# Performance work log

Measured on AMD Instinct MI355X. Metric: run time of the kernel, lower is better.

Reference implementation:

```python
import jax, jax.numpy as jnp
import numpy as np

B, S, IN, H, OUT, L = 64, 512, 512, 1024, 512, 2


def setup_inputs() -> dict:
    key = jax.random.key(0)
    ks = jax.random.split(key, 12)
    s_in = 1.0 / np.sqrt(IN)
    s_h = 1.0 / np.sqrt(H)
    inp = {
        "x": jax.random.normal(ks[0], (B, S, IN), dtype=jnp.float32),
        "h0": jnp.zeros((B, L, H), dtype=jnp.float32),
        # layer 0: gates stacked [z; r; g] along first axis
        "Wx0": jax.random.uniform(ks[1], (3 * H, IN), minval=-s_in, maxval=s_in),
        "Wh0": jax.random.uniform(ks[2], (3 * H, H), minval=-s_h, maxval=s_h),
        "bh0": jax.random.uniform(ks[3], (3 * H,), minval=-s_h, maxval=s_h),
        # layer 1 (input dim is H)
        "Wx1": jax.random.uniform(ks[4], (3 * H, H), minval=-s_h, maxval=s_h),
        "Wh1": jax.random.uniform(ks[5], (3 * H, H), minval=-s_h, maxval=s_h),
        "bh1": jax.random.uniform(ks[6], (3 * H,), minval=-s_h, maxval=s_h),
        # output projection fc_hy
        "Why": jax.random.uniform(ks[7], (OUT, H), minval=-s_h, maxval=s_h),
        "by": jax.random.uniform(ks[8], (OUT,), minval=-s_h, maxval=s_h),
    }
    return inp


def _gru_layer(x, h_init, Wx, Wh, bh):
    """x: [B,S,D], h_init: [B,H]. Returns (ys [B,S,H], h_final [B,H])."""
    # Batch the input-side projections for all timesteps at once.
    xp = jnp.einsum("bsd,gd->bsg", x, Wx)  # [B,S,3H]
    xz, xr, xg = jnp.split(xp, 3, axis=-1)
    Whz, Whr, Whg = jnp.split(Wh, 3, axis=0)
    bhz, bhr, bhg = jnp.split(bh, 3, axis=0)

    def step(h, xs):
        xz_t, xr_t, xg_t = xs  # each [B,H]
        z = jax.nn.sigmoid(xz_t + h @ Whz.T + bhz)
        r = jax.nn.sigmoid(xr_t + h @ Whr.T + bhr)
        g = jnp.tanh(xg_t + (r * h) @ Whg.T + bhg)
        h_new = z * h + (1.0 - z) * g
        return h_new, h_new

    # time-major scan
    xs = (xz.transpose(1, 0, 2), xr.transpose(1, 0, 2), xg.transpose(1, 0, 2))
    h_final, ys = jax.lax.scan(step, h_init, xs)
    return ys.transpose(1, 0, 2), h_final  # [B,S,H], [B,H]


def reference(x, h0, Wx0, Wh0, bh0, Wx1, Wh1, bh1, Why, by):
    # dropout rate is 0 -> dropout is identity
    y0, hf0 = _gru_layer(x, h0[:, 0, :], Wx0, Wh0, bh0)
    y1, hf1 = _gru_layer(y0, h0[:, 1, :], Wx1, Wh1, bh1)
    layer_output = jnp.einsum("bsh,oh->bso", y1, Why) + by  # [B,S,OUT]
    hidden_state = jnp.stack([hf0, hf1], axis=1)  # [B,L,H]
    return layer_output, jax.lax.stop_gradient(hidden_state)
```

## Files before the change

kernel.cpp:

```cpp
#include <hip/hip_runtime.h>
#include <hip/hip_bf16.h>

#define B_   64
#define S_   512
#define IN_  512
#define H_   1024
#define OUT_ 512
#define H3_  3072
#define TC_  32
#define TCL2 5
#define NCHUNK (S_ / TC_)
#define MC_  (B_ * TC_)
#define NROW (B_ * S_)

#define NBLK 512
#define NTHR 128
#define EXN  32768
#define FPAD 16
#define STAGE_OFF 0
#define HOWN_OFF  32768
#define ZOWN_OFF  33920
#define SMEM_BYTES 35072

typedef float f32x4 __attribute__((ext_vector_type(4)));
typedef short bf16x8 __attribute__((ext_vector_type(8)));
typedef unsigned int u32;
typedef u32 u32x4 __attribute__((ext_vector_type(4)));

struct ChainArgs {
  const float* xp;
  const __hip_bfloat16* Wh;
  float* hf;
  u32* hbuf;
  u32* rhbuf;
  u32* fA;
  u32* fB;
  __hip_bfloat16* y;
  u32 baseA, baseB;
  int t0;
  int layer;
  int active;
  int stagger;
};

__device__ __forceinline__ u32 f2bf_bits(float v) {
  union { __hip_bfloat16 b; unsigned short s; } cv;
  cv.b = __float2bfloat16(v);
  return (u32)cv.s;
}

__device__ __forceinline__ void coh_st(u32* p, u32 v) {
  __hip_atomic_store(p, v, __ATOMIC_RELAXED, __HIP_MEMORY_SCOPE_AGENT);
}
__device__ __forceinline__ u32 coh_ld(const u32* p) {
  return __hip_atomic_load(p, __ATOMIC_RELAXED, __HIP_MEMORY_SCOPE_AGENT);
}

__device__ __forceinline__ void waitflags(const u32* f, int rgbase, u32 target) {
  const u32* my = f + (size_t)(rgbase + (threadIdx.x & 63)) * FPAD;
  int it = 0;
  while (true) {
    u32 v = coh_ld(my);
    if (__all((int)(v >= target))) break;
    if (it < 2) {
      __builtin_amdgcn_s_sleep(2);
    } else {
      __builtin_amdgcn_s_sleep(8);
    }
    ++it;
  }
  __builtin_amdgcn_sched_barrier(0);
}

__device__ __forceinline__ void stage_ex(const u32* __restrict__ src, char* stage, int tid,
                                         int rg) {
  u32x4 v[16];
#pragma unroll
  for (int i = 0; i < 16; ++i) {
    int c4 = tid + i * NTHR;
    int cgp = c4 >> 5;
    int s = c4 & 31;
    const u32* p = src + (((size_t)(cgp * 4 + rg) * 16 + (s >> 1)) * 8 + (s & 1) * 4);
    asm volatile("global_load_dwordx4 %0, %1, off sc0 sc1" : "=v"(v[i]) : "v"(p));
  }
  asm volatile("s_waitcnt vmcnt(0)" ::: "memory");
#pragma unroll
  for (int i = 0; i < 16; ++i) {
    int c4 = tid + i * NTHR;
    int cgp = c4 >> 5;
    int s = c4 & 31;
    int r = s >> 1;
    *(u32x4*)(stage + r * 2048 + (((cgp * 32 + (s & 1) * 16)) ^ ((r & 7) << 4))) = v[i];
  }
}

__global__ __launch_bounds__(256) void cast_f32_to_bf16(const float* __restrict__ in,
                                                        __hip_bfloat16* __restrict__ out,
                                                        int n4) {
  int i = blockIdx.x * 256 + threadIdx.x;
  if (i >= n4) return;
  float4 v = ((const float4*)in)[i];
  out[4 * i + 0] = __float2bfloat16(v.x);
  out[4 * i + 1] = __float2bfloat16(v.y);
  out[4 * i + 2] = __float2bfloat16(v.z);
  out[4 * i + 3] = __float2bfloat16(v.w);
}

__global__ __launch_bounds__(256) void gather_cast_x(const float* __restrict__ x,
                                                     __hip_bfloat16* __restrict__ out, int t0) {
  int i = blockIdx.x * 256 + threadIdx.x;
  int e = i * 4;
  int b = e >> 14;
  int rem = e & 16383;
  float4 v = *(const float4*)(x + (size_t)b * (S_ * IN_) + (size_t)t0 * IN_ + rem);
  out[e + 0] = __float2bfloat16(v.x);
  out[e + 1] = __float2bfloat16(v.y);
  out[e + 2] = __float2bfloat16(v.z);
  out[e + 3] = __float2bfloat16(v.w);
}

template <bool REMAP>
__global__ __launch_bounds__(256) void gemm_nt_bias(const __hip_bfloat16* __restrict__ A,
                                                    const __hip_bfloat16* __restrict__ Bm,
                                                    const float* __restrict__ bias,
                                                    float* __restrict__ C, int M, int N, int K,
                                                    int t0) {
  const int lane = threadIdx.x & 63;
  const int w = threadIdx.x >> 6;
  const int wr = w >> 1, wc = w & 1;
  const int row0 = blockIdx.y * 128 + wr * 64;
  const int col0 = blockIdx.x * 128 + wc * 64;
  const int kl = (lane >> 4) * 8;
  const int m16 = lane & 15;
  f32x4 acc[4][4] = {};
  for (int k0 = 0; k0 < K; k0 += 32) {
    bf16x8 a[4], b[4];
#pragma unroll
    for (int i = 0; i < 4; ++i)
      a[i] = *(const bf16x8*)(A + (size_t)(row0 + i * 16 + m16) * K + k0 + kl);
#pragma unroll
    for (int j = 0; j < 4; ++j)
      b[j] = *(const bf16x8*)(Bm + (size_t)(col0 + j * 16 + m16) * K + k0 + kl);
#pragma unroll
    for (int i = 0; i < 4; ++i)
#pragma unroll
      for (int j = 0; j < 4; ++j)
        acc[i][j] = __builtin_amdgcn_mfma_f32_16x16x32_bf16(a[i], b[j], acc[i][j], 0, 0, 0);
  }
  const int rsub = (lane >> 4) * 4;
#pragma unroll
  for (int i = 0; i < 4; ++i) {
    int row = row0 + i * 16 + rsub;
#pragma unroll
    for (int j = 0; j < 4; ++j) {
      int col = col0 + j * 16 + m16;
      float bv = bias[col];
#pragma unroll
      for (int r = 0; r < 4; ++r) {
        int rr = row + r;
        int crow = REMAP ? ((rr >> TCL2) * S_ + t0 + (rr & (TC_ - 1))) : rr;
        C[(size_t)crow * N + col] = acc[i][j][r] + bv;
      }
    }
  }
}

__device__ __forceinline__ void chain_scan(const ChainArgs& ca, const float* __restrict__ h0,
                                           float* __restrict__ hid_out, char* smem, int bx) {
  char* stage = smem + STAGE_OFF;
  float* h_own = (float*)(smem + HOWN_OFF);
  float* z_own = (float*)(smem + ZOWN_OFF);

  const int tid = threadIdx.x;
  const int lane = tid & 63;
  const int w = tid >> 6;
  const int rg = bx >> 6;
  const int cg = bx & 63;
  const int fid = bx;
  const int rgbase = rg * 64;
  const int m16 = lane & 15;
  const int kl = (lane >> 4) * 8;
  const int rsub = (lane >> 4) * 4;
  const int swzA = (m16 & 7) << 4;

  const float* xp = ca.xp;
  const __hip_bfloat16* Wh = ca.Wh;
  u32* hbuf = ca.hbuf;
  u32* rhbuf = ca.rhbuf;
  u32* flagA = ca.fA;
  u32* flagB = ca.fB;
  const u32 baseA = ca.baseA, baseB = ca.baseB;
  const int t0 = ca.t0, layer = ca.layer;

  for (int i = 0; i < ca.stagger; ++i) __builtin_amdgcn_s_sleep(16);

  {
    int row = tid >> 3, pp = tid & 7;
    int col = cg * 16 + pp * 2;
    int grow = rg * 16 + row;
    float v0, v1;
    if (t0 == 0) {
      v0 = h0[((size_t)grow * 2 + layer) * H_ + col];
      v1 = h0[((size_t)grow * 2 + layer) * H_ + col + 1];
      coh_st(hbuf + EXN + (((size_t)(cg * 4 + rg) * 16 + row) * 8 + pp),
             f2bf_bits(v0) | (f2bf_bits(v1) << 16));
    } else {
      v0 = ca.hf[grow * H_ + col];
      v1 = ca.hf[grow * H_ + col + 1];
    }
    h_own[row * 17 + pp * 2] = v0;
    h_own[row * 17 + pp * 2 + 1] = v1;
  }
  asm volatile("s_waitcnt vmcnt(0)" ::: "memory");
  __syncthreads();
  if (tid == 0) coh_st(flagB + (size_t)fid * FPAD, baseB + 1);

  for (int t = 0; t < TC_; ++t) {
    const int par = t & 1;
    const int colA = cg * 16 + m16 + ((w == 1) ? H_ : 0);
    float xpv[4], xpg[4];
#pragma unroll
    for (int j = 0; j < 4; ++j) {
      int grow = rg * 16 + rsub + j;
      xpv[j] = xp[((size_t)(grow * TC_ + t)) * H3_ + colA];
    }
    if (w == 0) {
#pragma unroll
      for (int j = 0; j < 4; ++j) {
        int grow = rg * 16 + rsub + j;
        xpg[j] = xp[((size_t)(grow * TC_ + t)) * H3_ + 2 * H_ + cg * 16 + m16];
      }
    }

    waitflags(flagB, rgbase, baseB + 1 + t);
    stage_ex(hbuf + (par ^ 1) * EXN, stage, tid, rg);
    __syncthreads();
    {
      f32x4 acc0 = {}, acc1 = {};
      const char* abase = stage + m16 * 2048;
      const __hip_bfloat16* Bb = Wh + (size_t)colA * H_;
#pragma unroll
      for (int k0 = 0; k0 < H_; k0 += 64) {
        bf16x8 a0 = *(const bf16x8*)(abase + (((k0 + kl) * 2) ^ swzA));
        bf16x8 a1 = *(const bf16x8*)(abase + (((k0 + 32 + kl) * 2) ^ swzA));
        bf16x8 b0 = *(const bf16x8*)(Bb + k0 + kl);
        bf16x8 b1 = *(const bf16x8*)(Bb + k0 + 32 + kl);
        acc0 = __builtin_amdgcn_mfma_f32_16x16x32_bf16(a0, b0, acc0, 0, 0, 0);
        acc1 = __builtin_amdgcn_mfma_f32_16x16x32_bf16(a1, b1, acc1, 0, 0, 0);
      }
      if (w == 0) {
#pragma unroll
        for (int j = 0; j < 4; ++j) {
          float pre = acc0[j] + acc1[j] + xpv[j];
          z_own[(rsub + j) * 17 + m16] = 1.f / (1.f + expf(-pre));
        }
      } else {
#pragma unroll
        for (int j = 0; j < 4; ++j) {
          int lr = rsub + j;
          float pre = acc0[j] + acc1[j] + xpv[j];
          float s = 1.f / (1.f + expf(-pre));
          float rh = s * h_own[lr * 17 + m16];
          u32 bits = f2bf_bits(rh);
          u32 pair = bits | (((u32)__shfl_down((int)bits, 1)) << 16);
          if ((m16 & 1) == 0)
            coh_st(rhbuf + par * EXN + (((size_t)(cg * 4 + rg) * 16 + lr) * 8 + (m16 >> 1)),
                   pair);
        }
        asm volatile("s_waitcnt vmcnt(0)" ::: "memory");
      }
    }
    __syncthreads();
    if (tid == 0) coh_st(flagA + (size_t)fid * FPAD, baseA + t + 1);

    waitflags(flagA, rgbase, baseA + t + 1);
    stage_ex(rhbuf + par * EXN, stage, tid, rg);
    __syncthreads();
    if (w == 0) {
      f32x4 acc0 = {}, acc1 = {};
      const char* abase = stage + m16 * 2048;
      const __hip_bfloat16* Bb = Wh + (size_t)(2 * H_ + cg * 16 + m16) * H_;
#pragma unroll
      for (int k0 = 0; k0 < H_; k0 += 64) {
        bf16x8 a0 = *(const bf16x8*)(abase + (((k0 + kl) * 2) ^ swzA));
        bf16x8 a1 = *(const bf16x8*)(abase + (((k0 + 32 + kl) * 2) ^ swzA));
        bf16x8 b0 = *(const bf16x8*)(Bb + k0 + kl);
        bf16x8 b1 = *(const bf16x8*)(Bb + k0 + 32 + kl);
        acc0 = __builtin_amdgcn_mfma_f32_16x16x32_bf16(a0, b0, acc0, 0, 0, 0);
        acc1 = __builtin_amdgcn_mfma_f32_16x16x32_bf16(a1, b1, acc1, 0, 0, 0);
      }
#pragma unroll
      for (int j = 0; j < 4; ++j) {
        int lr = rsub + j;
        float pre = acc0[j] + acc1[j] + xpg[j];
        float gg = tanhf(pre);
        float zz = z_own[lr * 17 + m16];
        float hv = h_own[lr * 17 + m16];
        float hn = zz * hv + (1.f - zz) * gg;
        h_own[lr * 17 + m16] = hn;
        u32 bits = f2bf_bits(hn);
        u32 pair = bits | (((u32)__shfl_down((int)bits, 1)) << 16);
        if ((m16 & 1) == 0)
          coh_st(hbuf + par * EXN + (((size_t)(cg * 4 + rg) * 16 + lr) * 8 + (m16 >> 1)), pair);
        ca.y[((size_t)((rg * 16 + lr) * TC_ + t)) * H_ + cg * 16 + m16] = __float2bfloat16(hn);
      }
      asm volatile("s_waitcnt vmcnt(0)" ::: "memory");
    }
    __syncthreads();
    if (tid == 0) coh_st(flagB + (size_t)fid * FPAD, baseB + t + 2);
  }

  {
    int row = tid >> 3, pp = tid & 7;
    int col = cg * 16 + pp * 2;
    int grow = rg * 16 + row;
    float v0 = h_own[row * 17 + pp * 2];
    float v1 = h_own[row * 17 + pp * 2 + 1];
    ca.hf[grow * H_ + col] = v0;
    ca.hf[grow * H_ + col + 1] = v1;
    if (t0 + TC_ == S_) {
      hid_out[((size_t)grow * 2 + layer) * H_ + col] = v0;
      hid_out[((size_t)grow * 2 + layer) * H_ + col + 1] = v1;
    }
  }
}

__global__ __launch_bounds__(NTHR) void gru_scan_fused(ChainArgs a0, ChainArgs a1,
                                                       const float* __restrict__ h0,
                                                       float* __restrict__ hid_out) {
  extern __shared__ char smem[];
  if (blockIdx.x < 256) {
    if (!a0.active) return;
    chain_scan(a0, h0, hid_out, smem, blockIdx.x);
  } else {
    if (!a1.active) return;
    chain_scan(a1, h0, hid_out, smem, blockIdx.x - 256);
  }
}

extern "C" void kernel_launch(void* const* d_in, const int* in_sizes, int n_in,
                              void* d_out, int out_size, void* d_ws, size_t ws_size,
                              hipStream_t stream) {
  const float* x   = (const float*)d_in[0];
  const float* h0  = (const float*)d_in[1];
  const float* Wx0 = (const float*)d_in[2];
  const float* Wh0 = (const float*)d_in[3];
  const float* bh0 = (const float*)d_in[4];
  const float* Wx1 = (const float*)d_in[5];
  const float* Wh1 = (const float*)d_in[6];
  const float* bh1 = (const float*)d_in[7];
  const float* Why = (const float*)d_in[8];
  const float* by  = (const float*)d_in[9];
  float* out = (float*)d_out;
  float* hid_out = out + (size_t)NROW * OUT_;

  (void)hipFuncSetAttribute((const void*)gru_scan_fused,
                            hipFuncAttributeMaxDynamicSharedMemorySize, SMEM_BYTES);

  char* ws = (char*)d_ws;
  size_t off = 0;
  auto alloc = [&](size_t bytes) {
    char* p = ws + off;
    off += (bytes + 255) & ~(size_t)255;
    return p;
  };
  __hip_bfloat16* wx0b = (__hip_bfloat16*)alloc((size_t)H3_ * IN_ * 2);
  __hip_bfloat16* wh0b = (__hip_bfloat16*)alloc((size_t)H3_ * H_ * 2);
  __hip_bfloat16* wx1b = (__hip_bfloat16*)alloc((size_t)H3_ * H_ * 2);
  __hip_bfloat16* wh1b = (__hip_bfloat16*)alloc((size_t)H3_ * H_ * 2);
  __hip_bfloat16* whyb = (__hip_bfloat16*)alloc((size_t)OUT_ * H_ * 2);
  float* h_f32_0 = (float*)alloc((size_t)B_ * H_ * 4);
  float* h_f32_1 = (float*)alloc((size_t)B_ * H_ * 4);
  u32* hbuf_0  = (u32*)alloc((size_t)2 * EXN * 4);
  u32* hbuf_1  = (u32*)alloc((size_t)2 * EXN * 4);
  u32* rhbuf_0 = (u32*)alloc((size_t)2 * EXN * 4);
  u32* rhbuf_1 = (u32*)alloc((size_t)2 * EXN * 4);
  __hip_bfloat16* x_bfc = (__hip_bfloat16*)alloc((size_t)MC_ * IN_ * 2);
  __hip_bfloat16* y0buf = (__hip_bfloat16*)alloc((size_t)MC_ * H_ * 2);
  __hip_bfloat16* y1buf = (__hip_bfloat16*)alloc((size_t)MC_ * H_ * 2);
  float* xp0buf = (float*)alloc((size_t)MC_ * H3_ * 4);
  float* xp1buf = (float*)alloc((size_t)MC_ * H3_ * 4);
  u32* flags    = (u32*)alloc(4 * 256 * FPAD * 4);
  (void)ws_size;

  (void)hipMemsetAsync(flags, 0, 4 * 256 * FPAD * 4, stream);

  auto cast = [&](const float* in, __hip_bfloat16* o, size_t n) {
    cast_f32_to_bf16<<<dim3((unsigned)((n / 4 + 255) / 256)), dim3(256), 0, stream>>>(in, o,
                                                                                     (int)(n / 4));
  };
  cast(Wx0, wx0b, (size_t)H3_ * IN_);
  cast(Wh0, wh0b, (size_t)H3_ * H_);
  cast(Wx1, wx1b, (size_t)H3_ * H_);
  cast(Wh1, wh1b, (size_t)H3_ * H_);
  cast(Why, whyb, (size_t)OUT_ * H_);

  u32* fA0 = flags;
  u32* fB0 = flags + 256 * FPAD;
  u32* fA1 = flags + 512 * FPAD;
  u32* fB1 = flags + 768 * FPAD;

  auto mkchain = [&](int layer, int chunk, int active) {
    ChainArgs ca;
    int cc = chunk < 0 ? 0 : chunk;
    ca.xp = layer == 0 ? xp0buf : xp1buf;
    ca.Wh = layer == 0 ? wh0b : wh1b;
    ca.hf = layer == 0 ? h_f32_0 : h_f32_1;
    ca.hbuf = layer == 0 ? hbuf_0 : hbuf_1;
    ca.rhbuf = layer == 0 ? rhbuf_0 : rhbuf_1;
    ca.fA = layer == 0 ? fA0 : fA1;
    ca.fB = layer == 0 ? fB0 : fB1;
    ca.y = layer == 0 ? y0buf : y1buf;
    ca.baseA = (u32)cc * TC_;
    ca.baseB = (u32)cc * (TC_ + 1);
    ca.t0 = cc * TC_;
    ca.layer = layer;
    ca.active = active;
    ca.stagger = (layer == 1) ? 14 : 0;
    return ca;
  };

  gather_cast_x<<<dim3(MC_ * IN_ / 4 / 256), dim3(256), 0, stream>>>(x, x_bfc, 0);
  gemm_nt_bias<false><<<dim3(H3_ / 128, MC_ / 128), dim3(256), 0, stream>>>(
      x_bfc, wx0b, bh0, xp0buf, MC_, H3_, IN_, 0);

  for (int c = 0; c <= NCHUNK; ++c) {
    ChainArgs a0 = mkchain(0, c, c < NCHUNK ? 1 : 0);
    ChainArgs a1 = mkchain(1, c - 1, c > 0 ? 1 : 0);
    {
      void* args[] = {(void*)&a0, (void*)&a1, (void*)&h0, (void*)&hid_out};
      hipError_t e = hipLaunchCooperativeKernel((void*)gru_scan_fused, dim3(NBLK), dim3(NTHR),
                                                args, SMEM_BYTES, stream);
      if (e != hipSuccess) {
        (void)hipGetLastError();
        gru_scan_fused<<<dim3(NBLK), dim3(NTHR), SMEM_BYTES, stream>>>(a0, a1, h0, hid_out);
      }
    }
    if (c < NCHUNK) {
      gemm_nt_bias<false><<<dim3(H3_ / 128, MC_ / 128), dim3(256), 0, stream>>>(
          y0buf, wx1b, bh1, xp1buf, MC_, H3_, H_, 0);
    }
    if (c + 1 < NCHUNK) {
      gather_cast_x<<<dim3(MC_ * IN_ / 4 / 256), dim3(256), 0, stream>>>(x, x_bfc, (c + 1) * TC_);
      gemm_nt_bias<false><<<dim3(H3_ / 128, MC_ / 128), dim3(256), 0, stream>>>(
          x_bfc, wx0b, bh0, xp0buf, MC_, H3_, IN_, 0);
    }
    if (c > 0) {
      gemm_nt_bias<true><<<dim3(OUT_ / 128, MC_ / 128), dim3(256), 0, stream>>>(
          y1buf, whyb, by, out, MC_, OUT_, H_, (c - 1) * TC_);
    }
  }
}
```

Before: 10.59 ms.

## Consolidate GRU scan into fewer, wider blocks with 64 columns each

Each scan block now owns 64 hidden columns with 8 waves (4 z-gate, 4 r-gate) instead of 16 columns with 2 waves, so 128 blocks replace 512. This cuts the number of cross-block flags each step must poll from 64 to 16 per row group, and amortises staging of the shared hidden state across more columns per block. The exchange buffer layout, staging loop and flag indexing are rewritten to match. In exchange, only 128 CUs are used per step and each block carries more MFMA work serially.

```diff
diff --git a/kernel.cpp b/kernel.cpp
--- a/kernel.cpp
+++ b/kernel.cpp
@@ -13,14 +13,14 @@
 #define MC_  (B_ * TC_)
 #define NROW (B_ * S_)
 
-#define NBLK 512
-#define NTHR 128
+#define NBLK 128
+#define NTHR 512
 #define EXN  32768
 #define FPAD 16
 #define STAGE_OFF 0
 #define HOWN_OFF  32768
-#define ZOWN_OFF  33920
-#define SMEM_BYTES 35072
+#define ZOWN_OFF  36928
+#define SMEM_BYTES 41088
 
 typedef float f32x4 __attribute__((ext_vector_type(4)));
 typedef short bf16x8 __attribute__((ext_vector_type(8)));
@@ -57,7 +57,7 @@
 }
 
 __device__ __forceinline__ void waitflags(const u32* f, int rgbase, u32 target) {
-  const u32* my = f + (size_t)(rgbase + (threadIdx.x & 63)) * FPAD;
+  const u32* my = f + (size_t)(rgbase + (threadIdx.x & 15)) * FPAD;
   int it = 0;
   while (true) {
     u32 v = coh_ld(my);
@@ -74,23 +74,23 @@
 
 __device__ __forceinline__ void stage_ex(const u32* __restrict__ src, char* stage, int tid,
                                          int rg) {
-  u32x4 v[16];
-#pragma unroll
-  for (int i = 0; i < 16; ++i) {
+  u32x4 v[4];
+#pragma unroll
+  for (int i = 0; i < 4; ++i) {
     int c4 = tid + i * NTHR;
-    int cgp = c4 >> 5;
-    int s = c4 & 31;
-    const u32* p = src + (((size_t)(cgp * 4 + rg) * 16 + (s >> 1)) * 8 + (s & 1) * 4);
+    int cgp = c4 >> 7;
+    int s = c4 & 127;
+    const u32* p = src + (((size_t)(cgp * 4 + rg) * 16 + (s >> 3)) * 32 + (s & 7) * 4);
     asm volatile("global_load_dwordx4 %0, %1, off sc0 sc1" : "=v"(v[i]) : "v"(p));
   }
   asm volatile("s_waitcnt vmcnt(0)" ::: "memory");
 #pragma unroll
-  for (int i = 0; i < 16; ++i) {
+  for (int i = 0; i < 4; ++i) {
     int c4 = tid + i * NTHR;
-    int cgp = c4 >> 5;
-    int s = c4 & 31;
-    int r = s >> 1;
-    *(u32x4*)(stage + r * 2048 + (((cgp * 32 + (s & 1) * 16)) ^ ((r & 7) << 4))) = v[i];
+    int cgp = c4 >> 7;
+    int s = c4 & 127;
+    int r = s >> 3;
+    *(u32x4*)(stage + r * 2048 + ((cgp * 128 + (s & 7) * 16) ^ ((r & 7) << 4))) = v[i];
   }
 }
 
@@ -174,14 +174,17 @@
   const int tid = threadIdx.x;
   const int lane = tid & 63;
   const int w = tid >> 6;
-  const int rg = bx >> 6;
-  const int cg = bx & 63;
+  const int wc = w & 3;
+  const int isR = w >> 2;
+  const int rg = bx >> 4;
+  const int cg = bx & 15;
   const int fid = bx;
-  const int rgbase = rg * 64;
+  const int rgbase = rg * 16;
   const int m16 = lane & 15;
   const int kl = (lane >> 4) * 8;
   const int rsub = (lane >> 4) * 4;
   const int swzA = (m16 & 7) << 4;
+  const int cloc = wc * 16 + m16;
 
   const float* xp = ca.xp;
   const __hip_bfloat16* Wh = ca.Wh;
@@ -195,21 +198,21 @@
   for (int i = 0; i < ca.stagger; ++i) __builtin_amdgcn_s_sleep(16);
 
   {
-    int row = tid >> 3, pp = tid & 7;
-    int col = cg * 16 + pp * 2;
+    int row = tid >> 5, pp = tid & 31;
+    int col = cg * 64 + pp * 2;
     int grow = rg * 16 + row;
     float v0, v1;
     if (t0 == 0) {
       v0 = h0[((size_t)grow * 2 + layer) * H_ + col];
       v1 = h0[((size_t)grow * 2 + layer) * H_ + col + 1];
-      coh_st(hbuf + EXN + (((size_t)(cg * 4 + rg) * 16 + row) * 8 + pp),
+      coh_st(hbuf + EXN + (((size_t)(cg * 4 + rg) * 16 + row) * 32 + pp),
              f2bf_bits(v0) | (f2bf_bits(v1) << 16));
     } else {
       v0 = ca.hf[grow * H_ + col];
       v1 = ca.hf[grow * H_ + col + 1];
     }
-    h_own[row * 17 + pp * 2] = v0;
-    h_own[row * 17 + pp * 2 + 1] = v1;
+    h_own[row * 65 + pp * 2] = v0;
+    h_own[row * 65 + pp * 2 + 1] = v1;
   }
   asm volatile("s_waitcnt vmcnt(0)" ::: "memory");
   __syncthreads();
@@ -217,18 +220,18 @@
 
   for (int t = 0; t < TC_; ++t) {
     const int par = t & 1;
-    const int colA = cg * 16 + m16 + ((w == 1) ? H_ : 0);
+    const int colA = cg * 64 + cloc + (isR ? H_ : 0);
     float xpv[4], xpg[4];
 #pragma unroll
     for (int j = 0; j < 4; ++j) {
       int grow = rg * 16 + rsub + j;
       xpv[j] = xp[((size_t)(grow * TC_ + t)) * H3_ + colA];
     }
-    if (w == 0) {
+    if (w < 4) {
 #pragma unroll
       for (int j = 0; j < 4; ++j) {
         int grow = rg * 16 + rsub + j;
-        xpg[j] = xp[((size_t)(grow * TC_ + t)) * H3_ + 2 * H_ + cg * 16 + m16];
+        xpg[j] = xp[((size_t)(grow * TC_ + t)) * H3_ + 2 * H_ + cg * 64 + cloc];
       }
     }
 
@@ -248,11 +251,11 @@
         acc0 = __builtin_amdgcn_mfma_f32_16x16x32_bf16(a0, b0, acc0, 0, 0, 0);
         acc1 = __builtin_amdgcn_mfma_f32_16x16x32_bf16(a1, b1, acc1, 0, 0, 0);
       }
-      if (w == 0) {
+      if (!isR) {
 #pragma unroll
         for (int j = 0; j < 4; ++j) {
           float pre = acc0[j] + acc1[j] + xpv[j];
-          z_own[(rsub + j) * 17 + m16] = 1.f / (1.f + expf(-pre));
+          z_own[(rsub + j) * 65 + cloc] = 1.f / (1.f + expf(-pre));
         }
       } else {
 #pragma unroll
@@ -260,11 +263,11 @@
           int lr = rsub + j;
           float pre = acc0[j] + acc1[j] + xpv[j];
           float s = 1.f / (1.f + expf(-pre));
-          float rh = s * h_own[lr * 17 + m16];
+          float rh = s * h_own[lr * 65 + cloc];
           u32 bits = f2bf_bits(rh);
           u32 pair = bits | (((u32)__shfl_down((int)bits, 1)) << 16);
           if ((m16 & 1) == 0)
-            coh_st(rhbuf + par * EXN + (((size_t)(cg * 4 + rg) * 16 + lr) * 8 + (m16 >> 1)),
+            coh_st(rhbuf + par * EXN + (((size_t)(cg * 4 + rg) * 16 + lr) * 32 + (cloc >> 1)),
                    pair);
         }
         asm volatile("s_waitcnt vmcnt(0)" ::: "memory");
@@ -276,10 +279,10 @@
     waitflags(flagA, rgbase, baseA + t + 1);
     stage_ex(rhbuf + par * EXN, stage, tid, rg);
     __syncthreads();
-    if (w == 0) {
+    if (w < 4) {
       f32x4 acc0 = {}, acc1 = {};
       const char* abase = stage + m16 * 2048;
-      const __hip_bfloat16* Bb = Wh + (size_t)(2 * H_ + cg * 16 + m16) * H_;
+      const __hip_bfloat16* Bb = Wh + (size_t)(2 * H_ + cg * 64 + cloc) * H_;
 #pragma unroll
       for (int k0 = 0; k0 < H_; k0 += 64) {
         bf16x8 a0 = *(const bf16x8*)(abase + (((k0 + kl) * 2) ^ swzA));
@@ -294,15 +297,15 @@
         int lr = rsub + j;
         float pre = acc0[j] + acc1[j] + xpg[j];
         float gg = tanhf(pre);
-        float zz = z_own[lr * 17 + m16];
-        float hv = h_own[lr * 17 + m16];
+        float zz = z_own[lr * 65 + cloc];
+        float hv = h_own[lr * 65 + cloc];
         float hn = zz * hv + (1.f - zz) * gg;
-        h_own[lr * 17 + m16] = hn;
+        h_own[lr * 65 + cloc] = hn;
         u32 bits = f2bf_bits(hn);
         u32 pair = bits | (((u32)__shfl_down((int)bits, 1)) << 16);
         if ((m16 & 1) == 0)
-          coh_st(hbuf + par * EXN + (((size_t)(cg * 4 + rg) * 16 + lr) * 8 + (m16 >> 1)), pair);
-        ca.y[((size_t)((rg * 16 + lr) * TC_ + t)) * H_ + cg * 16 + m16] = __float2bfloat16(hn);
+          coh_st(hbuf + par * EXN + (((size_t)(cg * 4 + rg) * 16 + lr) * 32 + (cloc >> 1)), pair);
+        ca.y[((size_t)((rg * 16 + lr) * TC_ + t)) * H_ + cg * 64 + cloc] = __float2bfloat16(hn);
       }
       asm volatile("s_waitcnt vmcnt(0)" ::: "memory");
     }
@@ -311,11 +314,11 @@
   }
 
   {
-    int row = tid >> 3, pp = tid & 7;
-    int col = cg * 16 + pp * 2;
+    int row = tid >> 5, pp = tid & 31;
+    int col = cg * 64 + pp * 2;
     int grow = rg * 16 + row;
-    float v0 = h_own[row * 17 + pp * 2];
-    float v1 = h_own[row * 17 + pp * 2 + 1];
+    float v0 = h_own[row * 65 + pp * 2];
+    float v1 = h_own[row * 65 + pp * 2 + 1];
     ca.hf[grow * H_ + col] = v0;
     ca.hf[grow * H_ + col + 1] = v1;
     if (t0 + TC_ == S_) {
@@ -329,12 +332,12 @@
                                                        const float* __restrict__ h0,
                                                        float* __restrict__ hid_out) {
   extern __shared__ char smem[];
-  if (blockIdx.x < 256) {
+  if (blockIdx.x < 64) {
     if (!a0.active) return;
     chain_scan(a0, h0, hid_out, smem, blockIdx.x);
   } else {
     if (!a1.active) return;
-    chain_scan(a1, h0, hid_out, smem, blockIdx.x - 256);
+    chain_scan(a1, h0, hid_out, smem, blockIdx.x - 64);
   }
 }
 
```

Result: slower. 10.82 ms (+2.2%).
